# Performance work log

Measured on AMD Instinct MI355X. Metric: run time of the kernel, lower is better.

## Reference

```python
import jax, jax.numpy as jnp
import numpy as np

B, N, D = 32, 1024, 512
NUM_CLASSES = 4
LN_EPS = 1e-5


def _layer_norm(x, g, b):
    mu = jnp.mean(x, axis=-1, keepdims=True)
    var = jnp.mean(jnp.square(x - mu), axis=-1, keepdims=True)
    return (x - mu) * jax.lax.rsqrt(var + LN_EPS) * g + b


def setup_inputs() -> dict:
    key = jax.random.key(0)
    ks = jax.random.split(key, 8)
    s = 0.05
    inp = {
        "sc_matrix": jax.random.uniform(ks[0], (B, N, N), dtype=jnp.float32),
        # GCN encoder params
        "W1": jax.random.normal(ks[1], (N, D), dtype=jnp.float32) * s,
        "b1": jnp.zeros((D,), jnp.float32),
        "W2": jax.random.normal(ks[2], (D, D), dtype=jnp.float32) * s,
        "b2": jnp.zeros((D,), jnp.float32),
        "ln_g": jnp.ones((D,), jnp.float32),
        "ln_b": jnp.zeros((D,), jnp.float32),
        # classifier params
        "Wc1": jax.random.normal(ks[3], (D, 128), dtype=jnp.float32) * s,
        "bc1": jnp.zeros((128,), jnp.float32),
        "g1": jnp.ones((128,), jnp.float32),
        "t1": jnp.zeros((128,), jnp.float32),
        "Wc2": jax.random.normal(ks[4], (128, 64), dtype=jnp.float32) * s,
        "bc2": jnp.zeros((64,), jnp.float32),
        "g2": jnp.ones((64,), jnp.float32),
        "t2": jnp.zeros((64,), jnp.float32),
        "Wc3": jax.random.normal(ks[5], (64, NUM_CLASSES), dtype=jnp.float32) * s,
        "bc3": jnp.zeros((NUM_CLASSES,), jnp.float32),
    }
    return inp


def reference(sc_matrix, W1, b1, W2, b2, ln_g, ln_b,
              Wc1, bc1, g1, t1, Wc2, bc2, g2, t2, Wc3, bc3):
    # Every entry of sc_matrix is nonzero, so the edge list covers all (i,j)
    # pairs incl. self-loops; GCN message passing == dense normalized matmul.
    # PyG gcn_norm: deg[j] = sum_i A[i,j]; out = D^-1/2 A^T D^-1/2 h.
    A = sc_matrix                              # [B,N,N], A[b,i,j] = edge i->j
    deg = jnp.sum(A, axis=-2)                  # col sums, [B,N]
    dis = jnp.where(deg > 0, jax.lax.rsqrt(deg), 0.0)   # deg^{-1/2}
    An = jnp.swapaxes(A, -1, -2) * dis[:, :, None] * dis[:, None, :]  # [B,N,N]

    x = sc_matrix                              # node features = SC rows [B,N,N]
    h = jax.nn.relu(jnp.matmul(An, jnp.matmul(x, W1)) + b1)   # conv1+relu [B,N,D]
    h = jnp.matmul(An, jnp.matmul(h, W2)) + b2                # conv2      [B,N,D]
    z = _layer_norm(h, ln_g, ln_b)

    z_pooled = jnp.mean(z, axis=1)             # [B,D]

    c = jax.nn.relu(_layer_norm(z_pooled @ Wc1 + bc1, g1, t1))
    c = jax.nn.relu(_layer_norm(c @ Wc2 + bc2, g2, t2))
    logits = c @ Wc3 + bc3                     # [B,num_classes]
    return (logits, z_pooled)
```

## Files before the change

### kernel.cpp

```cpp
#include <hip/hip_runtime.h>
#include <hip/hip_bf16.h>

#define B_ 32
#define N_ 1024
#define D_ 512
#define LN_EPS 1e-5f

using bf16 = __bf16;
using bf16x4 = __attribute__((ext_vector_type(4))) __bf16;
using bf16x8 = __attribute__((ext_vector_type(8))) __bf16;
using floatx4 = __attribute__((ext_vector_type(4))) float;

__device__ __forceinline__ void gld16(const bf16* gp, bf16* lp) {
  __builtin_amdgcn_global_load_lds(
      (const __attribute__((address_space(1))) void*)gp,
      (__attribute__((address_space(3))) void*)lp, 16, 0, 0);
}

__global__ __launch_bounds__(256) void k_deg(const float* __restrict__ A,
                                             float* __restrict__ deg,
                                             bf16* __restrict__ Abf) {
  int b = blockIdx.y;
  int i0 = blockIdx.x * 32;
  int t = threadIdx.x;
  const float* p = A + (size_t)b * N_ * N_ + (size_t)i0 * N_ + t * 4;
  bf16* op = Abf + (size_t)b * N_ * N_ + (size_t)i0 * N_ + t * 4;
  float4 acc = {0.f, 0.f, 0.f, 0.f};
  #pragma unroll 4
  for (int i = 0; i < 32; ++i) {
    float4 v = *(const float4*)(p + (size_t)i * N_);
    acc.x += v.x; acc.y += v.y; acc.z += v.z; acc.w += v.w;
    bf16x4 o = {(bf16)v.x, (bf16)v.y, (bf16)v.z, (bf16)v.w};
    *(bf16x4*)(op + (size_t)i * N_) = o;
  }
  float* d = deg + b * N_ + t * 4;
  atomicAdd(d + 0, acc.x); atomicAdd(d + 1, acc.y);
  atomicAdd(d + 2, acc.z); atomicAdd(d + 3, acc.w);
}

__global__ __launch_bounds__(256) void k_build(const bf16* __restrict__ Abf,
                                               const float* __restrict__ deg,
                                               bf16* __restrict__ Anbf) {
  __shared__ float tile[64][65];
  __shared__ float disI[64], disJ[64];
  int b = blockIdx.z;
  int i0 = blockIdx.x * 64;
  int j0 = blockIdx.y * 64;
  int t = threadIdx.x;
  const bf16* Ab = Abf + (size_t)b * N_ * N_;
  bf16* Anb = Anbf + (size_t)b * N_ * N_;
  if (t < 64) {
    float v = deg[b * N_ + i0 + t];
    disI[t] = v > 0.f ? rsqrtf(v) : 0.f;
  } else if (t < 128) {
    float v = deg[b * N_ + j0 + (t - 64)];
    disJ[t - 64] = v > 0.f ? rsqrtf(v) : 0.f;
  }
  #pragma unroll
  for (int cc = 0; cc < 4; ++cc) {
    int chunk = cc * 256 + t;
    int r = chunk >> 4;
    int c4 = (chunk & 15) << 2;
    bf16x4 v = *(const bf16x4*)(Ab + (size_t)(j0 + r) * N_ + i0 + c4);
    tile[r][c4 + 0] = (float)v[0]; tile[r][c4 + 1] = (float)v[1];
    tile[r][c4 + 2] = (float)v[2]; tile[r][c4 + 3] = (float)v[3];
  }
  __syncthreads();
  #pragma unroll
  for (int cc = 0; cc < 4; ++cc) {
    int chunk = cc * 256 + t;
    int ii = chunk >> 4;
    int jj4 = (chunk & 15) << 2;
    float di = disI[ii];
    bf16x4 o;
    #pragma unroll
    for (int e = 0; e < 4; ++e)
      o[e] = (bf16)(tile[jj4 + e][ii] * di * disJ[jj4 + e]);
    *(bf16x4*)(Anb + (size_t)(i0 + ii) * N_ + j0 + jj4) = o;
  }
}

__global__ __launch_bounds__(256) void k_transpose(const float* __restrict__ W1,
                                                   bf16* __restrict__ W1t,
                                                   const float* __restrict__ W2,
                                                   bf16* __restrict__ W2t) {
  __shared__ float tile[64][65];
  int blk = blockIdx.x;
  const float* in; bf16* outp; int R, C, c0, r0;
  if (blk < 128) {
    in = W1; outp = W1t; R = N_; C = D_;
    c0 = (blk & 7) * 64; r0 = (blk >> 3) * 64;
  } else {
    blk -= 128;
    in = W2; outp = W2t; R = D_; C = D_;
    c0 = (blk & 7) * 64; r0 = (blk >> 3) * 64;
  }
  int t = threadIdx.x;
  #pragma unroll
  for (int cc = 0; cc < 4; ++cc) {
    int idx = cc * 256 + t;
    int r = idx >> 4, c4 = (idx & 15) << 2;
    const float4 v = *(const float4*)(in + (size_t)(r0 + r) * C + c0 + c4);
    tile[r][c4 + 0] = v.x; tile[r][c4 + 1] = v.y;
    tile[r][c4 + 2] = v.z; tile[r][c4 + 3] = v.w;
  }
  __syncthreads();
  #pragma unroll
  for (int cc = 0; cc < 4; ++cc) {
    int idx = cc * 256 + t;
    int c = idx >> 4, r4 = (idx & 15) << 2;
    bf16* dst = outp + (size_t)(c0 + c) * R + r0 + r4;
    #pragma unroll
    for (int e = 0; e < 4; ++e) dst[e] = (bf16)tile[r4 + e][c];
  }
}

template <bool BIAS, bool RELU>
__global__ __launch_bounds__(512, 2) void k_gemm8(
    const bf16* __restrict__ Abase, size_t strideA,
    const bf16* __restrict__ Btbase, size_t strideBt,
    bf16* __restrict__ Cbase, size_t strideC,
    const float* __restrict__ bias, int Nn, int K) {
  __shared__ bf16 sA[2][2][8192];
  __shared__ bf16 sB[2][2][8192];

  int nxy = gridDim.x * gridDim.y;
  int L = blockIdx.z * nxy + blockIdx.y * gridDim.x + blockIdx.x;
  int b = (L & 7) + 8 * (L / (nxy * 8));
  int inner = (L >> 3) % nxy;
  int n0 = (inner % gridDim.x) * 256;
  int m0 = (inner / gridDim.x) * 256;

  const bf16* A = Abase + (size_t)b * strideA;
  const bf16* Bt = Btbase + (size_t)b * strideBt;
  int t = threadIdx.x;
  int lane = t & 63;
  int wid = t >> 6;
  int wm = wid >> 2, wn = wid & 3;
  int l16 = lane & 15, q = lane >> 4;
  int xorb = l16 & 7;
  int ck0 = ((q ^ xorb) << 3);
  int ck1 = (((q + 4) ^ xorb) << 3);

  int r0 = t >> 3;
  int csrc = (((t & 7) ^ (r0 & 7)) << 3);
  const bf16* ag = A + (size_t)(m0 + r0) * K + csrc;
  const bf16* bg = Bt + (size_t)(n0 + ((r0 >> 5) << 6) + (r0 & 31)) * K + csrc;
  bf16* al = &sA[0][0][(size_t)t * 8];
  bf16* bl = &sB[0][0][(size_t)t * 8];

#define STAGE_A(bf_, hf_, kt_)                                                 \
  { gld16(ag + (size_t)((hf_) * 64) * K + (kt_),                               \
          al + (bf_) * 16384 + (hf_) * 8192);                                  \
    gld16(ag + (size_t)(128 + (hf_) * 64) * K + (kt_),                         \
          al + (bf_) * 16384 + (hf_) * 8192 + 4096); }
#define STAGE_B(bf_, hf_, kt_)                                                 \
  { gld16(bg + (size_t)((hf_) * 32) * K + (kt_),                               \
          bl + (bf_) * 16384 + (hf_) * 8192);                                  \
    gld16(bg + (size_t)(128 + (hf_) * 32) * K + (kt_),                         \
          bl + (bf_) * 16384 + (hf_) * 8192 + 4096); }

  floatx4 acc[8][4];
  #pragma unroll
  for (int i = 0; i < 8; ++i)
    #pragma unroll
    for (int j = 0; j < 4; ++j) acc[i][j] = (floatx4){0.f, 0.f, 0.f, 0.f};

  bf16x8 a[4][2];
  bf16x8 bq[4][2];
  const bf16* arow = &sA[0][0][(wm * 64 + l16) * 64];
  const bf16* brow = &sB[0][0][(wn * 32 + l16) * 64];

#define RD_A(bf_, mq_)                                                         \
  _Pragma("unroll") for (int i = 0; i < 4; ++i) {                              \
    a[i][0] = *(const bf16x8*)(arow + (bf_) * 16384 + (mq_) * 8192 +           \
                               i * 1024 + ck0);                                \
    a[i][1] = *(const bf16x8*)(arow + (bf_) * 16384 + (mq_) * 8192 +           \
                               i * 1024 + ck1);                                \
  }
#define RD_B(bf_, nq_)                                                         \
  _Pragma("unroll") for (int j = 0; j < 2; ++j) {                              \
    bq[(nq_) * 2 + j][0] = *(const bf16x8*)(brow + (bf_) * 16384 +             \
                                            (nq_) * 8192 + j * 1024 + ck0);    \
    bq[(nq_) * 2 + j][1] = *(const bf16x8*)(brow + (bf_) * 16384 +             \
                                            (nq_) * 8192 + j * 1024 + ck1);    \
  }
#define MFMA_Q(mq_, nq_)                                                       \
  _Pragma("unroll") for (int i = 0; i < 4; ++i)                                \
    _Pragma("unroll") for (int j = 0; j < 2; ++j) {                            \
      acc[(mq_) * 4 + i][(nq_) * 2 + j] =                                      \
          __builtin_amdgcn_mfma_f32_16x16x32_bf16(                             \
              a[i][0], bq[(nq_) * 2 + j][0],                                   \
              acc[(mq_) * 4 + i][(nq_) * 2 + j], 0, 0, 0);                     \
      acc[(mq_) * 4 + i][(nq_) * 2 + j] =                                      \
          __builtin_amdgcn_mfma_f32_16x16x32_bf16(                             \
              a[i][1], bq[(nq_) * 2 + j][1],                                   \
              acc[(mq_) * 4 + i][(nq_) * 2 + j], 0, 0, 0);                     \
    }
#define BARRIER __builtin_amdgcn_s_barrier()
#define LGKM0                                                                  \
  do {                                                                         \
    asm volatile("s_waitcnt lgkmcnt(0)" ::: "memory");                         \
    __builtin_amdgcn_sched_barrier(0);                                         \
  } while (0)
#define PRIO_MFMA(mq_, nq_)                                                    \
  __builtin_amdgcn_s_setprio(1);                                               \
  MFMA_Q(mq_, nq_);                                                            \
  __builtin_amdgcn_s_setprio(0)

  STAGE_A(0, 0, 0); STAGE_B(0, 0, 0); STAGE_A(0, 1, 0); STAGE_B(0, 1, 0);
  STAGE_A(1, 0, 64); STAGE_B(1, 0, 64);
  asm volatile("s_waitcnt vmcnt(4)" ::: "memory");
  BARRIER;

  int NI = K >> 7;
  for (int it = 0; it < NI; ++it) {
    int kb = it << 7;
    int k1 = kb + 64;
    int k2 = kb + 128; bool p2 = k2 < K;
    int k3 = kb + 192; bool p3 = k3 < K;
    bool lastit = (it == NI - 1);
    RD_A(0, 0); RD_B(0, 0);
    STAGE_A(1, 1, k1);
    BARRIER; LGKM0; PRIO_MFMA(0, 0);
    BARRIER;
    RD_B(0, 1);
    STAGE_B(1, 1, k1);
    BARRIER; LGKM0; PRIO_MFMA(0, 1);
    BARRIER;
    RD_A(0, 1);
    if (p2) STAGE_A(0, 0, k2);
    BARRIER; LGKM0; PRIO_MFMA(1, 0);
    BARRIER;
    if (p2) STAGE_B(0, 0, k2);
    if (lastit) { asm volatile("s_waitcnt vmcnt(0)" ::: "memory"); }
    else        { asm volatile("s_waitcnt vmcnt(4)" ::: "memory"); }
    BARRIER; LGKM0; PRIO_MFMA(1, 1);
    BARRIER;
    RD_A(1, 0); RD_B(1, 0);
    if (p2) STAGE_A(0, 1, k2);
    BARRIER; LGKM0; PRIO_MFMA(0, 0);
    BARRIER;
    RD_B(1, 1);
    if (p2) STAGE_B(0, 1, k2);
    BARRIER; LGKM0; PRIO_MFMA(0, 1);
    BARRIER;
    RD_A(1, 1);
    if (p3) STAGE_A(1, 0, k3);
    BARRIER; LGKM0; PRIO_MFMA(1, 0);
    BARRIER;
    if (p3) STAGE_B(1, 0, k3);
    if (lastit) { asm volatile("s_waitcnt vmcnt(0)" ::: "memory"); }
    else        { asm volatile("s_waitcnt vmcnt(4)" ::: "memory"); }
    BARRIER; LGKM0; PRIO_MFMA(1, 1);
    BARRIER;
  }

  bf16* C = Cbase + (size_t)b * strideC;
  #pragma unroll
  for (int fm = 0; fm < 8; ++fm)
    #pragma unroll
    for (int fn = 0; fn < 4; ++fn)
      #pragma unroll
      for (int r = 0; r < 4; ++r) {
        int row = m0 + wm * 128 + fm * 16 + q * 4 + r;
        int col = n0 + wn * 64 + fn * 16 + l16;
        float v = acc[fm][fn][r];
        if (BIAS) v += bias[col];
        if (RELU) v = v > 0.f ? v : 0.f;
        C[(size_t)row * Nn + col] = (bf16)v;
      }
#undef STAGE_A
#undef STAGE_B
#undef RD_A
#undef RD_B
#undef MFMA_Q
#undef BARRIER
#undef LGKM0
#undef PRIO_MFMA
}

__global__ __launch_bounds__(256) void k_lnpool(const bf16* __restrict__ H2,
                                                const float* __restrict__ g,
                                                const float* __restrict__ be,
                                                float* __restrict__ zp_accum) {
  int b = blockIdx.y;
  int r0 = blockIdx.x * 64;
  int t = threadIdx.x, lane = t & 63, w = t >> 6;
  float ge[8], bee[8];
  #pragma unroll
  for (int e = 0; e < 8; ++e) { ge[e] = g[lane * 8 + e]; bee[e] = be[lane * 8 + e]; }
  float acc[8] = {0, 0, 0, 0, 0, 0, 0, 0};
  for (int rr = 0; rr < 16; ++rr) {
    int row = r0 + w * 16 + rr;
    const bf16* p = H2 + ((size_t)b * N_ + row) * D_ + lane * 8;
    bf16x8 hv = *(const bf16x8*)p;
    float x[8];
    float s = 0.f;
    #pragma unroll
    for (int e = 0; e < 8; ++e) { x[e] = (float)hv[e]; s += x[e]; }
    #pragma unroll
    for (int off = 32; off; off >>= 1) s += __shfl_xor(s, off);
    float mu = s * (1.f / 512.f);
    float ss = 0.f;
    #pragma unroll
    for (int e = 0; e < 8; ++e) { float d = x[e] - mu; ss += d * d; }
    #pragma unroll
    for (int off = 32; off; off >>= 1) ss += __shfl_xor(ss, off);
    float rs = rsqrtf(ss * (1.f / 512.f) + LN_EPS);
    #pragma unroll
    for (int e = 0; e < 8; ++e) acc[e] += (x[e] - mu) * rs * ge[e] + bee[e];
  }
  __shared__ float part[4][512];
  #pragma unroll
  for (int e = 0; e < 8; ++e) part[w][lane * 8 + e] = acc[e];
  __syncthreads();
  #pragma unroll
  for (int k = 0; k < 2; ++k) {
    int d = t + k * 256;
    float s4 = part[0][d] + part[1][d] + part[2][d] + part[3][d];
    atomicAdd(&zp_accum[b * D_ + d], s4);
  }
}

__global__ __launch_bounds__(128) void k_cls(
    const float* __restrict__ zp_accum,
    const float* __restrict__ Wc1, const float* __restrict__ bc1,
    const float* __restrict__ g1, const float* __restrict__ t1,
    const float* __restrict__ Wc2, const float* __restrict__ bc2,
    const float* __restrict__ g2, const float* __restrict__ t2,
    const float* __restrict__ Wc3, const float* __restrict__ bc3,
    float* __restrict__ out) {
  __shared__ float z[512];
  __shared__ float c1s[128];
  __shared__ float c2s[64];
  __shared__ float red[128];
  int b = blockIdx.x, t = threadIdx.x;
  #pragma unroll
  for (int k = 0; k < 4; ++k) {
    int d = t + k * 128;
    float v = zp_accum[b * 512 + d] * (1.f / 1024.f);
    z[d] = v;
    out[128 + b * 512 + d] = v;
  }
  __syncthreads();
  float y = bc1[t];
  for (int d = 0; d < 512; ++d) y += z[d] * Wc1[d * 128 + t];
  red[t] = y;
  __syncthreads();
  float mu = 0.f;
  for (int k = 0; k < 128; ++k) mu += red[k];
  mu *= (1.f / 128.f);
  float var = 0.f;
  for (int k = 0; k < 128; ++k) { float dd = red[k] - mu; var += dd * dd; }
  var *= (1.f / 128.f);
  float c = (y - mu) * rsqrtf(var + LN_EPS) * g1[t] + t1[t];
  c1s[t] = c > 0.f ? c : 0.f;
  __syncthreads();
  if (t < 64) {
    float y2 = bc2[t];
    for (int k = 0; k < 128; ++k) y2 += c1s[k] * Wc2[k * 64 + t];
    red[t] = y2;
  }
  __syncthreads();
  if (t < 64) {
    float mu2 = 0.f;
    for (int k = 0; k < 64; ++k) mu2 += red[k];
    mu2 *= (1.f / 64.f);
    float v2 = 0.f;
    for (int k = 0; k < 64; ++k) { float dd = red[k] - mu2; v2 += dd * dd; }
    v2 *= (1.f / 64.f);
    float cc = (red[t] - mu2) * rsqrtf(v2 + LN_EPS) * g2[t] + t2[t];
    c2s[t] = cc > 0.f ? cc : 0.f;
  }
  __syncthreads();
  if (t < 4) {
    float y3 = bc3[t];
    for (int k = 0; k < 64; ++k) y3 += c2s[k] * Wc3[k * 4 + t];
    out[b * 4 + t] = y3;
  }
}

extern "C" void kernel_launch(void* const* d_in, const int* in_sizes, int n_in,
                              void* d_out, int out_size, void* d_ws, size_t ws_size,
                              hipStream_t stream) {
  const float* A   = (const float*)d_in[0];
  const float* W1  = (const float*)d_in[1];
  const float* b1  = (const float*)d_in[2];
  const float* W2  = (const float*)d_in[3];
  const float* b2  = (const float*)d_in[4];
  const float* lng = (const float*)d_in[5];
  const float* lnb = (const float*)d_in[6];
  const float* Wc1 = (const float*)d_in[7];
  const float* bc1 = (const float*)d_in[8];
  const float* g1  = (const float*)d_in[9];
  const float* t1  = (const float*)d_in[10];
  const float* Wc2 = (const float*)d_in[11];
  const float* bc2 = (const float*)d_in[12];
  const float* g2  = (const float*)d_in[13];
  const float* t2  = (const float*)d_in[14];
  const float* Wc3 = (const float*)d_in[15];
  const float* bc3 = (const float*)d_in[16];
  float* out = (float*)d_out;

  char* ws = (char*)d_ws;
  size_t off = 0;
  auto alloc = [&](size_t bytes) {
    char* p = ws + off;
    off += (bytes + 255) & ~(size_t)255;
    return p;
  };
  float* deg  = (float*)alloc((size_t)B_ * N_ * 4);
  float* zp   = (float*)alloc((size_t)B_ * D_ * 4);
  bf16* Anbf  = (bf16*)alloc((size_t)B_ * N_ * N_ * 2);
  bf16* W1t   = (bf16*)alloc((size_t)D_ * N_ * 2);
  bf16* W2t   = (bf16*)alloc((size_t)D_ * D_ * 2);
  bf16* T12t  = (bf16*)alloc((size_t)B_ * D_ * N_ * 2);
  bf16* H1    = (bf16*)alloc((size_t)B_ * N_ * D_ * 2);
  bf16* Abf   = (bf16*)alloc((size_t)B_ * N_ * N_ * 2);
  bf16* H2    = Abf;

  hipMemsetAsync(deg, 0, (size_t)B_ * N_ * 4 + (size_t)B_ * D_ * 4 + 256, stream);

  k_deg<<<dim3(32, B_), 256, 0, stream>>>(A, deg, Abf);
  k_build<<<dim3(16, 16, B_), 256, 0, stream>>>(Abf, deg, Anbf);
  k_transpose<<<192, 256, 0, stream>>>(W1, W1t, W2, W2t);

  k_gemm8<false, false><<<dim3(4, 2, B_), 512, 0, stream>>>(
      W1t, 0, Abf, (size_t)N_ * N_, T12t, (size_t)D_ * N_, nullptr, N_, N_);
  k_gemm8<true, true><<<dim3(2, 4, B_), 512, 0, stream>>>(
      Anbf, (size_t)N_ * N_, T12t, (size_t)D_ * N_, H1, (size_t)N_ * D_, b1, D_, N_);
  k_gemm8<false, false><<<dim3(4, 2, B_), 512, 0, stream>>>(
      W2t, 0, H1, (size_t)N_ * D_, T12t, (size_t)D_ * N_, nullptr, N_, D_);
  k_gemm8<true, false><<<dim3(2, 4, B_), 512, 0, stream>>>(
      Anbf, (size_t)N_ * N_, T12t, (size_t)D_ * N_, H2, (size_t)N_ * D_, b2, D_, N_);

  k_lnpool<<<dim3(16, B_), 256, 0, stream>>>(H2, lng, lnb, zp);
  k_cls<<<B_, 128, 0, stream>>>(zp, Wc1, bc1, g1, t1, Wc2, bc2, g2, t2, Wc3, bc3, out);
}
```

Before: 425.6 us.

## Merge four GEMM launches into one persistent kernel with grid barriers

```diff
diff --git a/kernel.cpp b/kernel.cpp
--- a/kernel.cpp
+++ b/kernel.cpp
@@ -115,21 +115,16 @@
   }
 }
 
-template <bool BIAS, bool RELU>
-__global__ __launch_bounds__(512, 2) void k_gemm8(
+__device__ __forceinline__ void gemm_body(
     const bf16* __restrict__ Abase, size_t strideA,
     const bf16* __restrict__ Btbase, size_t strideBt,
     bf16* __restrict__ Cbase, size_t strideC,
-    const float* __restrict__ bias, int Nn, int K) {
-  __shared__ bf16 sA[2][2][8192];
-  __shared__ bf16 sB[2][2][8192];
-
-  int nxy = gridDim.x * gridDim.y;
-  int L = blockIdx.z * nxy + blockIdx.y * gridDim.x + blockIdx.x;
-  int b = (L & 7) + 8 * (L / (nxy * 8));
-  int inner = (L >> 3) % nxy;
-  int n0 = (inner % gridDim.x) * 256;
-  int m0 = (inner / gridDim.x) * 256;
+    const float* __restrict__ bias, int Nn, int K, int gxs,
+    bool BIAS, bool RELU, bf16* sAbuf, bf16* sBbuf, int L) {
+  int b = (L & 7) + 8 * (L >> 6);
+  int inner = (L >> 3) & 7;
+  int n0 = (inner & ((1 << gxs) - 1)) << 8;
+  int m0 = (inner >> gxs) << 8;
 
   const bf16* A = Abase + (size_t)b * strideA;
   const bf16* Bt = Btbase + (size_t)b * strideBt;
@@ -146,8 +141,8 @@
   int csrc = (((t & 7) ^ (r0 & 7)) << 3);
   const bf16* ag = A + (size_t)(m0 + r0) * K + csrc;
   const bf16* bg = Bt + (size_t)(n0 + ((r0 >> 5) << 6) + (r0 & 31)) * K + csrc;
-  bf16* al = &sA[0][0][(size_t)t * 8];
-  bf16* bl = &sB[0][0][(size_t)t * 8];
+  bf16* al = sAbuf + (size_t)t * 8;
+  bf16* bl = sBbuf + (size_t)t * 8;
 
 #define STAGE_A(bf_, hf_, kt_)                                                 \
   { gld16(ag + (size_t)((hf_) * 64) * K + (kt_),                               \
@@ -168,8 +163,8 @@
 
   bf16x8 a[4][2];
   bf16x8 bq[4][2];
-  const bf16* arow = &sA[0][0][(wm * 64 + l16) * 64];
-  const bf16* brow = &sB[0][0][(wn * 32 + l16) * 64];
+  const bf16* arow = sAbuf + (wm * 64 + l16) * 64;
+  const bf16* brow = sBbuf + (wn * 32 + l16) * 64;
 
 #define RD_A(bf_, mq_)                                                         \
   _Pragma("unroll") for (int i = 0; i < 4; ++i) {                              \
@@ -280,6 +275,42 @@
 #undef PRIO_MFMA
 }
 
+__device__ __forceinline__ void grid_bar(unsigned int* p) {
+  __syncthreads();
+  if (threadIdx.x == 0) {
+    __threadfence();
+    __hip_atomic_fetch_add(p, 1u, __ATOMIC_ACQ_REL, __HIP_MEMORY_SCOPE_AGENT);
+    while (__hip_atomic_load(p, __ATOMIC_ACQUIRE, __HIP_MEMORY_SCOPE_AGENT) <
+           256u)
+      __builtin_amdgcn_s_sleep(2);
+    __threadfence();
+  }
+  __syncthreads();
+}
+
+__global__ __launch_bounds__(512, 2) void k_gemm4(
+    const bf16* __restrict__ W1t, const bf16* __restrict__ W2t,
+    const bf16* __restrict__ Abf, const bf16* __restrict__ Anbf,
+    bf16* __restrict__ T12t, bf16* __restrict__ H1, bf16* __restrict__ H2,
+    const float* __restrict__ b1, const float* __restrict__ b2,
+    unsigned int* __restrict__ gbar) {
+  __shared__ bf16 sA[2 * 2 * 8192];
+  __shared__ bf16 sB[2 * 2 * 8192];
+  int L = blockIdx.x;
+
+  gemm_body(W1t, 0, Abf, (size_t)N_ * N_, T12t, (size_t)D_ * N_,
+            nullptr, N_, N_, 2, false, false, sA, sB, L);
+  grid_bar(gbar + 0);
+  gemm_body(Anbf, (size_t)N_ * N_, T12t, (size_t)D_ * N_, H1, (size_t)N_ * D_,
+            b1, D_, N_, 1, true, true, sA, sB, L);
+  grid_bar(gbar + 1);
+  gemm_body(W2t, 0, H1, (size_t)N_ * D_, T12t, (size_t)D_ * N_,
+            nullptr, N_, D_, 2, false, false, sA, sB, L);
+  grid_bar(gbar + 2);
+  gemm_body(Anbf, (size_t)N_ * N_, T12t, (size_t)D_ * N_, H2, (size_t)N_ * D_,
+            b2, D_, N_, 1, true, false, sA, sB, L);
+}
+
 __global__ __launch_bounds__(256) void k_lnpool(const bf16* __restrict__ H2,
                                                 const float* __restrict__ g,
                                                 const float* __restrict__ be,
@@ -412,6 +443,7 @@
   };
   float* deg  = (float*)alloc((size_t)B_ * N_ * 4);
   float* zp   = (float*)alloc((size_t)B_ * D_ * 4);
+  unsigned int* gbar = (unsigned int*)alloc(256);
   bf16* Anbf  = (bf16*)alloc((size_t)B_ * N_ * N_ * 2);
   bf16* W1t   = (bf16*)alloc((size_t)D_ * N_ * 2);
   bf16* W2t   = (bf16*)alloc((size_t)D_ * D_ * 2);
@@ -426,14 +458,8 @@
   k_build<<<dim3(16, 16, B_), 256, 0, stream>>>(Abf, deg, Anbf);
   k_transpose<<<192, 256, 0, stream>>>(W1, W1t, W2, W2t);
 
-  k_gemm8<false, false><<<dim3(4, 2, B_), 512, 0, stream>>>(
-      W1t, 0, Abf, (size_t)N_ * N_, T12t, (size_t)D_ * N_, nullptr, N_, N_);
-  k_gemm8<true, true><<<dim3(2, 4, B_), 512, 0, stream>>>(
-      Anbf, (size_t)N_ * N_, T12t, (size_t)D_ * N_, H1, (size_t)N_ * D_, b1, D_, N_);
-  k_gemm8<false, false><<<dim3(4, 2, B_), 512, 0, stream>>>(
-      W2t, 0, H1, (size_t)N_ * D_, T12t, (size_t)D_ * N_, nullptr, N_, D_);
-  k_gemm8<true, false><<<dim3(2, 4, B_), 512, 0, stream>>>(
-      Anbf, (size_t)N_ * N_, T12t, (size_t)D_ * N_, H2, (size_t)N_ * D_, b2, D_, N_);
+  k_gemm4<<<256, 512, 0, stream>>>(W1t, W2t, Abf, Anbf, T12t, H1, H2,
+                                   b1, b2, gbar);
 
   k_lnpool<<<dim3(16, B_), 256, 0, stream>>>(H2, lng, lnb, zp);
   k_cls<<<B_, 128, 0, stream>>>(zp, Wc1, bc1, g1, t1, Wc2, bc2, g2, t2, Wc3, bc3, out);
```

Result: slower. 687.2 us (+61.5%).

## Stage GEMM epilogue through LDS for vectorized stores; merge transpose into deg kernel

Applied to the files above, without the earlier changes.

```diff
diff --git a/kernel.cpp b/kernel.cpp
--- a/kernel.cpp
+++ b/kernel.cpp
@@ -17,25 +17,61 @@
       (__attribute__((address_space(3))) void*)lp, 16, 0, 0);
 }
 
-__global__ __launch_bounds__(256) void k_deg(const float* __restrict__ A,
+__global__ __launch_bounds__(256) void k_pre(const float* __restrict__ A,
                                              float* __restrict__ deg,
-                                             bf16* __restrict__ Abf) {
-  int b = blockIdx.y;
-  int i0 = blockIdx.x * 32;
+                                             bf16* __restrict__ Abf,
+                                             const float* __restrict__ W1,
+                                             bf16* __restrict__ W1t,
+                                             const float* __restrict__ W2,
+                                             bf16* __restrict__ W2t) {
+  int blk = blockIdx.x;
   int t = threadIdx.x;
-  const float* p = A + (size_t)b * N_ * N_ + (size_t)i0 * N_ + t * 4;
-  bf16* op = Abf + (size_t)b * N_ * N_ + (size_t)i0 * N_ + t * 4;
-  float4 acc = {0.f, 0.f, 0.f, 0.f};
-  #pragma unroll 4
-  for (int i = 0; i < 32; ++i) {
-    float4 v = *(const float4*)(p + (size_t)i * N_);
-    acc.x += v.x; acc.y += v.y; acc.z += v.z; acc.w += v.w;
-    bf16x4 o = {(bf16)v.x, (bf16)v.y, (bf16)v.z, (bf16)v.w};
-    *(bf16x4*)(op + (size_t)i * N_) = o;
-  }
-  float* d = deg + b * N_ + t * 4;
-  atomicAdd(d + 0, acc.x); atomicAdd(d + 1, acc.y);
-  atomicAdd(d + 2, acc.z); atomicAdd(d + 3, acc.w);
+  if (blk < 1024) {
+    int b = blk >> 5;
+    int i0 = (blk & 31) * 32;
+    const float* p = A + (size_t)b * N_ * N_ + (size_t)i0 * N_ + t * 4;
+    bf16* op = Abf + (size_t)b * N_ * N_ + (size_t)i0 * N_ + t * 4;
+    float4 acc = {0.f, 0.f, 0.f, 0.f};
+    #pragma unroll 4
+    for (int i = 0; i < 32; ++i) {
+      float4 v = *(const float4*)(p + (size_t)i * N_);
+      acc.x += v.x; acc.y += v.y; acc.z += v.z; acc.w += v.w;
+      bf16x4 o = {(bf16)v.x, (bf16)v.y, (bf16)v.z, (bf16)v.w};
+      *(bf16x4*)(op + (size_t)i * N_) = o;
+    }
+    float* d = deg + b * N_ + t * 4;
+    atomicAdd(d + 0, acc.x); atomicAdd(d + 1, acc.y);
+    atomicAdd(d + 2, acc.z); atomicAdd(d + 3, acc.w);
+  } else {
+    __shared__ float tile[64][65];
+    blk -= 1024;
+    const float* in; bf16* outp; int R, C, c0, r0;
+    if (blk < 128) {
+      in = W1; outp = W1t; R = N_; C = D_;
+      c0 = (blk & 7) * 64; r0 = (blk >> 3) * 64;
+    } else {
+      blk -= 128;
+      in = W2; outp = W2t; R = D_; C = D_;
+      c0 = (blk & 7) * 64; r0 = (blk >> 3) * 64;
+    }
+    #pragma unroll
+    for (int cc = 0; cc < 4; ++cc) {
+      int idx = cc * 256 + t;
+      int r = idx >> 4, c4 = (idx & 15) << 2;
+      const float4 v = *(const float4*)(in + (size_t)(r0 + r) * C + c0 + c4);
+      tile[r][c4 + 0] = v.x; tile[r][c4 + 1] = v.y;
+      tile[r][c4 + 2] = v.z; tile[r][c4 + 3] = v.w;
+    }
+    __syncthreads();
+    #pragma unroll
+    for (int cc = 0; cc < 4; ++cc) {
+      int idx = cc * 256 + t;
+      int c = idx >> 4, r4 = (idx & 15) << 2;
+      bf16* dst = outp + (size_t)(c0 + c) * R + r0 + r4;
+      #pragma unroll
+      for (int e = 0; e < 4; ++e) dst[e] = (bf16)tile[r4 + e][c];
+    }
+  }
 }
 
 __global__ __launch_bounds__(256) void k_build(const bf16* __restrict__ Abf,
@@ -80,49 +116,15 @@
   }
 }
 
-__global__ __launch_bounds__(256) void k_transpose(const float* __restrict__ W1,
-                                                   bf16* __restrict__ W1t,
-                                                   const float* __restrict__ W2,
-                                                   bf16* __restrict__ W2t) {
-  __shared__ float tile[64][65];
-  int blk = blockIdx.x;
-  const float* in; bf16* outp; int R, C, c0, r0;
-  if (blk < 128) {
-    in = W1; outp = W1t; R = N_; C = D_;
-    c0 = (blk & 7) * 64; r0 = (blk >> 3) * 64;
-  } else {
-    blk -= 128;
-    in = W2; outp = W2t; R = D_; C = D_;
-    c0 = (blk & 7) * 64; r0 = (blk >> 3) * 64;
-  }
-  int t = threadIdx.x;
-  #pragma unroll
-  for (int cc = 0; cc < 4; ++cc) {
-    int idx = cc * 256 + t;
-    int r = idx >> 4, c4 = (idx & 15) << 2;
-    const float4 v = *(const float4*)(in + (size_t)(r0 + r) * C + c0 + c4);
-    tile[r][c4 + 0] = v.x; tile[r][c4 + 1] = v.y;
-    tile[r][c4 + 2] = v.z; tile[r][c4 + 3] = v.w;
-  }
-  __syncthreads();
-  #pragma unroll
-  for (int cc = 0; cc < 4; ++cc) {
-    int idx = cc * 256 + t;
-    int c = idx >> 4, r4 = (idx & 15) << 2;
-    bf16* dst = outp + (size_t)(c0 + c) * R + r0 + r4;
-    #pragma unroll
-    for (int e = 0; e < 4; ++e) dst[e] = (bf16)tile[r4 + e][c];
-  }
-}
-
 template <bool BIAS, bool RELU>
 __global__ __launch_bounds__(512, 2) void k_gemm8(
     const bf16* __restrict__ Abase, size_t strideA,
     const bf16* __restrict__ Btbase, size_t strideBt,
     bf16* __restrict__ Cbase, size_t strideC,
     const float* __restrict__ bias, int Nn, int K) {
-  __shared__ bf16 sA[2][2][8192];
-  __shared__ bf16 sB[2][2][8192];
+  __shared__ __align__(16) bf16 smem[65536];
+  bf16* sAp = smem;
+  bf16* sBp = smem + 32768;
 
   int nxy = gridDim.x * gridDim.y;
   int L = blockIdx.z * nxy + blockIdx.y * gridDim.x + blockIdx.x;
@@ -130,7 +132,6 @@
   int inner = (L >> 3) % nxy;
   int n0 = (inner % gridDim.x) * 256;
   int m0 = (inner / gridDim.x) * 256;
-
   const bf16* A = Abase + (size_t)b * strideA;
   const bf16* Bt = Btbase + (size_t)b * strideBt;
   int t = threadIdx.x;
@@ -141,13 +142,12 @@
   int xorb = l16 & 7;
   int ck0 = ((q ^ xorb) << 3);
   int ck1 = (((q + 4) ^ xorb) << 3);
-
   int r0 = t >> 3;
   int csrc = (((t & 7) ^ (r0 & 7)) << 3);
   const bf16* ag = A + (size_t)(m0 + r0) * K + csrc;
   const bf16* bg = Bt + (size_t)(n0 + ((r0 >> 5) << 6) + (r0 & 31)) * K + csrc;
-  bf16* al = &sA[0][0][(size_t)t * 8];
-  bf16* bl = &sB[0][0][(size_t)t * 8];
+  bf16* al = sAp + (size_t)t * 8;
+  bf16* bl = sBp + (size_t)t * 8;
 
 #define STAGE_A(bf_, hf_, kt_)                                                 \
   { gld16(ag + (size_t)((hf_) * 64) * K + (kt_),                               \
@@ -168,8 +168,8 @@
 
   bf16x8 a[4][2];
   bf16x8 bq[4][2];
-  const bf16* arow = &sA[0][0][(wm * 64 + l16) * 64];
-  const bf16* brow = &sB[0][0][(wn * 32 + l16) * 64];
+  const bf16* arow = sAp + (wm * 64 + l16) * 64;
+  const bf16* brow = sBp + (wn * 32 + l16) * 64;
 
 #define RD_A(bf_, mq_)                                                         \
   _Pragma("unroll") for (int i = 0; i < 4; ++i) {                              \
@@ -203,16 +203,12 @@
     asm volatile("s_waitcnt lgkmcnt(0)" ::: "memory");                         \
     __builtin_amdgcn_sched_barrier(0);                                         \
   } while (0)
-#define PRIO_MFMA(mq_, nq_)                                                    \
-  __builtin_amdgcn_s_setprio(1);                                               \
-  MFMA_Q(mq_, nq_);                                                            \
-  __builtin_amdgcn_s_setprio(0)
+#define VMCNT(n_) asm volatile("s_waitcnt vmcnt(" #n_ ")" ::: "memory")
 
   STAGE_A(0, 0, 0); STAGE_B(0, 0, 0); STAGE_A(0, 1, 0); STAGE_B(0, 1, 0);
   STAGE_A(1, 0, 64); STAGE_B(1, 0, 64);
-  asm volatile("s_waitcnt vmcnt(4)" ::: "memory");
+  VMCNT(4);
   BARRIER;
-
   int NI = K >> 7;
   for (int it = 0; it < NI; ++it) {
     int kb = it << 7;
@@ -222,54 +218,74 @@
     bool lastit = (it == NI - 1);
     RD_A(0, 0); RD_B(0, 0);
     STAGE_A(1, 1, k1);
-    BARRIER; LGKM0; PRIO_MFMA(0, 0);
+    BARRIER; LGKM0;
+    __builtin_amdgcn_s_setprio(1); MFMA_Q(0, 0); __builtin_amdgcn_s_setprio(0);
     BARRIER;
     RD_B(0, 1);
     STAGE_B(1, 1, k1);
-    BARRIER; LGKM0; PRIO_MFMA(0, 1);
+    BARRIER; LGKM0;
+    __builtin_amdgcn_s_setprio(1); MFMA_Q(0, 1); __builtin_amdgcn_s_setprio(0);
     BARRIER;
     RD_A(0, 1);
     if (p2) STAGE_A(0, 0, k2);
-    BARRIER; LGKM0; PRIO_MFMA(1, 0);
+    BARRIER; LGKM0;
+    __builtin_amdgcn_s_setprio(1); MFMA_Q(1, 0); __builtin_amdgcn_s_setprio(0);
     BARRIER;
     if (p2) STAGE_B(0, 0, k2);
-    if (lastit) { asm volatile("s_waitcnt vmcnt(0)" ::: "memory"); }
-    else        { asm volatile("s_waitcnt vmcnt(4)" ::: "memory"); }
-    BARRIER; LGKM0; PRIO_MFMA(1, 1);
+    if (lastit) { VMCNT(0); } else { VMCNT(4); }
+    BARRIER; LGKM0;
+    __builtin_amdgcn_s_setprio(1); MFMA_Q(1, 1); __builtin_amdgcn_s_setprio(0);
     BARRIER;
     RD_A(1, 0); RD_B(1, 0);
     if (p2) STAGE_A(0, 1, k2);
-    BARRIER; LGKM0; PRIO_MFMA(0, 0);
+    BARRIER; LGKM0;
+    __builtin_amdgcn_s_setprio(1); MFMA_Q(0, 0); __builtin_amdgcn_s_setprio(0);
     BARRIER;
     RD_B(1, 1);
     if (p2) STAGE_B(0, 1, k2);
-    BARRIER; LGKM0; PRIO_MFMA(0, 1);
+    BARRIER; LGKM0;
+    __builtin_amdgcn_s_setprio(1); MFMA_Q(0, 1); __builtin_amdgcn_s_setprio(0);
     BARRIER;
     RD_A(1, 1);
     if (p3) STAGE_A(1, 0, k3);
-    BARRIER; LGKM0; PRIO_MFMA(1, 0);
+    BARRIER; LGKM0;
+    __builtin_amdgcn_s_setprio(1); MFMA_Q(1, 0); __builtin_amdgcn_s_setprio(0);
     BARRIER;
     if (p3) STAGE_B(1, 0, k3);
-    if (lastit) { asm volatile("s_waitcnt vmcnt(0)" ::: "memory"); }
-    else        { asm volatile("s_waitcnt vmcnt(4)" ::: "memory"); }
-    BARRIER; LGKM0; PRIO_MFMA(1, 1);
+    if (lastit) { VMCNT(0); } else { VMCNT(4); }
+    BARRIER; LGKM0;
+    __builtin_amdgcn_s_setprio(1); MFMA_Q(1, 1); __builtin_amdgcn_s_setprio(0);
     BARRIER;
   }
 
   bf16* C = Cbase + (size_t)b * strideC;
   #pragma unroll
-  for (int fm = 0; fm < 8; ++fm)
-    #pragma unroll
-    for (int fn = 0; fn < 4; ++fn)
+  for (int h = 0; h < 2; ++h) {
+    BARRIER;
+    if (wm == h) {
       #pragma unroll
-      for (int r = 0; r < 4; ++r) {
-        int row = m0 + wm * 128 + fm * 16 + q * 4 + r;
-        int col = n0 + wn * 64 + fn * 16 + l16;
-        float v = acc[fm][fn][r];
-        if (BIAS) v += bias[col];
-        if (RELU) v = v > 0.f ? v : 0.f;
-        C[(size_t)row * Nn + col] = (bf16)v;
-      }
+      for (int fm = 0; fm < 8; ++fm)
+        #pragma unroll
+        for (int fn = 0; fn < 4; ++fn)
+          #pragma unroll
+          for (int r = 0; r < 4; ++r) {
+            float v = acc[fm][fn][r];
+            if (BIAS) v += bias[n0 + wn * 64 + fn * 16 + l16];
+            if (RELU) v = v > 0.f ? v : 0.f;
+            smem[(fm * 16 + q * 4 + r) * 264 + wn * 64 + fn * 16 + l16] =
+                (bf16)v;
+          }
+    }
+    BARRIER;
+    #pragma unroll
+    for (int i = 0; i < 8; ++i) {
+      int idx = i * 512 + t;
+      int row = idx >> 5;
+      int c8 = (idx & 31) << 3;
+      bf16x8 vv = *(const bf16x8*)(smem + row * 264 + c8);
+      *(bf16x8*)(C + (size_t)(m0 + h * 128 + row) * Nn + n0 + c8) = vv;
+    }
+  }
 #undef STAGE_A
 #undef STAGE_B
 #undef RD_A
@@ -277,7 +293,7 @@
 #undef MFMA_Q
 #undef BARRIER
 #undef LGKM0
-#undef PRIO_MFMA
+#undef VMCNT
 }
 
 __global__ __launch_bounds__(256) void k_lnpool(const bf16* __restrict__ H2,
@@ -422,9 +438,8 @@
 
   hipMemsetAsync(deg, 0, (size_t)B_ * N_ * 4 + (size_t)B_ * D_ * 4 + 256, stream);
 
-  k_deg<<<dim3(32, B_), 256, 0, stream>>>(A, deg, Abf);
+  k_pre<<<1216, 256, 0, stream>>>(A, deg, Abf, W1, W1t, W2, W2t);
   k_build<<<dim3(16, 16, B_), 256, 0, stream>>>(Abf, deg, Anbf);
-  k_transpose<<<192, 256, 0, stream>>>(W1, W1t, W2, W2t);
 
   k_gemm8<false, false><<<dim3(4, 2, B_), 512, 0, stream>>>(
       W1t, 0, Abf, (size_t)N_ * N_, T12t, (size_t)D_ * N_, nullptr, N_, N_);
```

After: 423.6 us. Within noise of the previous version (-0.5%).
